# Performance work log

Measured on AMD Instinct MI355X. Metric: run time of the kernel, lower is better.

The kernel has to match this reference:

```python
import jax, jax.numpy as jnp
import numpy as np

IN_DIM = 256
OUT_DIM = 64   # per-head dim
NUM_HEADS = 8
B = 8
N = 1024


def setup_inputs() -> dict:
    key = jax.random.key(0)
    k_adj, k_h, kq, kk, kv, kbq, kbk, kbv = jax.random.split(key, 8)
    adj_matrix = jax.random.randint(k_adj, (N, N), 0, 2, dtype=jnp.int32)
    h = jax.random.normal(k_h, (B, N, IN_DIM), dtype=jnp.float32)
    s = 1.0 / np.sqrt(IN_DIM)
    Wq = jax.random.normal(kq, (IN_DIM, OUT_DIM * NUM_HEADS), dtype=jnp.float32) * s
    Wk = jax.random.normal(kk, (IN_DIM, OUT_DIM * NUM_HEADS), dtype=jnp.float32) * s
    Wv = jax.random.normal(kv, (IN_DIM, OUT_DIM * NUM_HEADS), dtype=jnp.float32) * s
    bq = jax.random.normal(kbq, (OUT_DIM * NUM_HEADS,), dtype=jnp.float32) * 0.01
    bk = jax.random.normal(kbk, (OUT_DIM * NUM_HEADS,), dtype=jnp.float32) * 0.01
    bv = jax.random.normal(kbv, (OUT_DIM * NUM_HEADS,), dtype=jnp.float32) * 0.01
    return {"adj_matrix": adj_matrix, "h": h, "Wq": Wq, "bq": bq,
            "Wk": Wk, "bk": bk, "Wv": Wv, "bv": bv}


def reference(adj_matrix, h, Wq, bq, Wk, bk, Wv, bv):
    B_, N_, _ = h.shape
    H, D = NUM_HEADS, OUT_DIM
    Qh = (h @ Wq + bq).reshape(B_, N_, H, D)
    Kh = (h @ Wk + bk).reshape(B_, N_, H, D)
    Vh = (h @ Wv + bv).reshape(B_, N_, H, D)
    scores = jnp.einsum('bnhd,bmhd->bhnm', Qh, Kh) / jnp.sqrt(jnp.float32(D))
    # adjacency mask broadcast over batch and heads (neigh_attention=True)
    scores = jnp.where(adj_matrix[None, None, :, :] == 0, -jnp.inf, scores)
    attn = jax.nn.softmax(scores, axis=-1)
    out = jnp.einsum('bhnm,bmhd->bnhd', attn, Vh)
    return out.reshape(B_, N_, H * D)
```

## Files before the change

### kernel.cpp

```cpp
#include <hip/hip_runtime.h>
#include <hip/hip_bf16.h>
#include <math.h>

#define IN_DIM 256
#define HD     512
#define NHEADS 8
#define DH     64
#define NSEQ   1024
#define BATCH  8

#define QSCALE 0.18033688011112042f

typedef unsigned short u16;
typedef unsigned int   u32;
typedef short bf16x8 __attribute__((ext_vector_type(8)));
typedef float f32x4  __attribute__((ext_vector_type(4)));
typedef float f32x16 __attribute__((ext_vector_type(16)));
typedef unsigned int u32x2 __attribute__((ext_vector_type(2)));

#if __has_builtin(__builtin_amdgcn_exp2f)
#define EXP2(x) __builtin_amdgcn_exp2f(x)
#else
#define EXP2(x) __expf(0.69314718056f * (x))
#endif

static __device__ __forceinline__ u16 f2bf(float x) {
    u32 u = __builtin_bit_cast(u32, x);
    u += 0x7FFFu + ((u >> 16) & 1u);
    return (u16)(u >> 16);
}
static __device__ __forceinline__ u32 pk(u16 a, u16 b) {
    return (u32)a | ((u32)b << 16);
}
static __device__ __forceinline__ u32 cvtpk(float a, float b) {
    __hip_bfloat162 t = __float22bfloat162_rn(make_float2(a, b));
    u32 r; __builtin_memcpy(&r, &t, 4);
    return r;
}
static __device__ __forceinline__ f32x16 maskinit(uint4 a, uint4 b) {
    f32x16 c;
    u32 ws[8] = {a.x, a.y, a.z, a.w, b.x, b.y, b.z, b.w};
#pragma unroll
    for (int i = 0; i < 8; ++i) {
        c[2 * i]     = __builtin_bit_cast(float, ws[i] << 16);
        c[2 * i + 1] = __builtin_bit_cast(float, ws[i] & 0xFFFF0000u);
    }
    return c;
}

static __device__ __forceinline__ void pswap(u32 &a, u32 &b) {
#if __has_builtin(__builtin_amdgcn_permlane32_swap)
    u32x2 r = __builtin_amdgcn_permlane32_swap(a, b, false, false);
    a = r.x; b = r.y;
#else
    const bool hi = (threadIdx.x & 32) != 0;
    u32 as = (u32)__shfl_xor((int)a, 32, 64);
    u32 bs = (u32)__shfl_xor((int)b, 32, 64);
    u32 na = hi ? bs : a;
    u32 nb = hi ? b  : as;
    a = na; b = nb;
#endif
}

#define MFMA32(a, b, c) __builtin_amdgcn_mfma_f32_32x32x16_bf16(a, b, c, 0, 0, 0)

#define GLOAD16(G, L)                                                          \
    __builtin_amdgcn_global_load_lds(                                          \
        (const __attribute__((address_space(1))) unsigned int*)(const void*)(G),\
        (__attribute__((address_space(3))) unsigned int*)(void*)(L), 16, 0, 0)

static __device__ __forceinline__ float sm_pack_half(const f32x16 st, bf16x8* pb) {
    float p[16];
#pragma unroll
    for (int r = 0; r < 16; ++r) p[r] = EXP2(st[r]);
    float t = (((p[0] + p[1]) + (p[2] + p[3])) + ((p[4] + p[5]) + (p[6] + p[7])))
            + (((p[8] + p[9]) + (p[10] + p[11])) + ((p[12] + p[13]) + (p[14] + p[15])));
    uint4 w0, w1;
    w0.x = cvtpk(p[0], p[1]);   w0.y = cvtpk(p[2], p[3]);
    w0.z = cvtpk(p[4], p[5]);   w0.w = cvtpk(p[6], p[7]);
    w1.x = cvtpk(p[8], p[9]);   w1.y = cvtpk(p[10], p[11]);
    w1.z = cvtpk(p[12], p[13]); w1.w = cvtpk(p[14], p[15]);
    pswap(w0.x, w1.x); pswap(w0.y, w1.y); pswap(w0.z, w1.z); pswap(w0.w, w1.w);
    pb[0] = __builtin_bit_cast(bf16x8, w0);
    pb[1] = __builtin_bit_cast(bf16x8, w1);
    return t;
}

__global__ __launch_bounds__(256)
void wtrans_kernel(const float* __restrict__ Wq, const float* __restrict__ Wk,
                   const float* __restrict__ Wv, u16* __restrict__ Wt)
{
    __shared__ float tile[64 * 65];
    const int bid = blockIdx.x, tid = threadIdx.x;
    const int k0 = (bid & 3) * 64, n0 = ((bid >> 2) & 7) * 64, wsel = bid >> 5;
    const float* W = (wsel == 0) ? Wq : (wsel == 1) ? Wk : Wv;
    u16* Out = Wt + (size_t)wsel * HD * IN_DIM;

    const int r = tid >> 2, c0 = (tid & 3) * 16;
#pragma unroll
    for (int j = 0; j < 16; j += 4) {
        float4 v = *(const float4*)(W + (size_t)(k0 + r) * HD + n0 + c0 + j);
        tile[r * 65 + c0 + j + 0] = v.x; tile[r * 65 + c0 + j + 1] = v.y;
        tile[r * 65 + c0 + j + 2] = v.z; tile[r * 65 + c0 + j + 3] = v.w;
    }
    __syncthreads();
    const int n = tid >> 2, ks = (tid & 3) * 16;
    u16 o[16];
#pragma unroll
    for (int j = 0; j < 16; ++j) o[j] = f2bf(tile[(ks + j) * 65 + n]);
    uint4 u0, u1;
    u0.x = pk(o[0], o[1]);   u0.y = pk(o[2], o[3]);
    u0.z = pk(o[4], o[5]);   u0.w = pk(o[6], o[7]);
    u1.x = pk(o[8], o[9]);   u1.y = pk(o[10], o[11]);
    u1.z = pk(o[12], o[13]); u1.w = pk(o[14], o[15]);
    u16* dst = Out + (size_t)(n0 + n) * IN_DIM + k0 + ks;
    *(uint4*)(dst) = u0;
    *(uint4*)(dst + 8) = u1;
}

__global__ __launch_bounds__(256, 4)
void gemm_mask_kernel(const float* __restrict__ h, const u16* __restrict__ Wt,
                      const int* __restrict__ adj,
                      const float* __restrict__ bq, const float* __restrict__ bk,
                      const float* __restrict__ bv,
                      u16* __restrict__ Qg, u16* __restrict__ Kg,
                      u16* __restrict__ Vtg, u16* __restrict__ Madd2)
{
    __shared__ u16 pool[64 * 64 + 3 * 64 * 64];
    const int tid = threadIdx.x;

    if (blockIdx.y >= 8) {
        int* tile = (int*)pool;
        const int abid = (blockIdx.y - 8) * 128 + blockIdx.x;
        const int tR = abid >> 4, tC = abid & 15;
        const int r = tid >> 2, cg = (tid & 3) * 16;
        const int* src = adj + (size_t)(tR * 64 + r) * NSEQ + tC * 64 + cg;
#pragma unroll
        for (int j = 0; j < 16; j += 4) {
            int4 a = *(const int4*)(src + j);
            tile[r * 65 + cg + j + 0] = a.x; tile[r * 65 + cg + j + 1] = a.y;
            tile[r * 65 + cg + j + 2] = a.z; tile[r * 65 + cg + j + 3] = a.w;
        }
        __syncthreads();
        const int q = tid >> 2, p0 = (tid & 3) * 16;
        u16 o[16];
#pragma unroll
        for (int j = 0; j < 16; ++j) {
            const int p = p0 + j;
            const int c = 32 * (p >> 5) + (p & 3) + 4 * ((p >> 4) & 1) + 8 * ((p >> 2) & 3);
            o[j] = (tile[q * 65 + c] == 0) ? (u16)0xFF7F : (u16)0;
        }
        uint4 u0, u1;
        u0.x = pk(o[0], o[1]);   u0.y = pk(o[2], o[3]);
        u0.z = pk(o[4], o[5]);   u0.w = pk(o[6], o[7]);
        u1.x = pk(o[8], o[9]);   u1.y = pk(o[10], o[11]);
        u1.z = pk(o[12], o[13]); u1.w = pk(o[14], o[15]);
        u16* dst = Madd2 + (size_t)(tR * 64 + q) * NSEQ + tC * 64 + p0;
        *(uint4*)(dst) = u0;
        *(uint4*)(dst + 8) = u1;
        return;
    }

    u16* As = pool;
    u16* Bs = pool + 64 * 64;

    const int m0 = blockIdx.x * 64;
    const int hh = blockIdx.y;
    const int n0 = hh * 64;

    const int w = tid >> 6, lane = tid & 63;
    const int l31 = lane & 31, half = lane >> 5;
    const int mh = w & 1, nh = w >> 1;
    const int s7 = l31 & 7;

    f32x16 acc[3] = {};

    const int arw = tid >> 2, acg = (tid & 3) * 2;
    const int brw = tid & 63, bgrp = tid >> 6;
    const float* srcA = h + (size_t)(m0 + arw) * IN_DIM;

    for (int kk = 0; kk < IN_DIM; kk += 64) {
        __syncthreads();
#pragma unroll
        for (int g = 0; g < 2; ++g) {
            const float* p = srcA + kk + (acg + g) * 8;
            float4 v0 = *(const float4*)(p);
            float4 v1 = *(const float4*)(p + 4);
            uint4 u;
            u.x = cvtpk(v0.x, v0.y); u.y = cvtpk(v0.z, v0.w);
            u.z = cvtpk(v1.x, v1.y); u.w = cvtpk(v1.z, v1.w);
            *(uint4*)&As[arw * 64 + (((acg + g) ^ (arw & 7)) * 8)] = u;
        }
#pragma unroll
        for (int i = 0; i < 6; ++i) {
            const int gc = bgrp * 6 + i;
            const int wh = gc >> 3, c8 = gc & 7;
            *(uint4*)&Bs[wh * 4096 + brw * 64 + ((c8 ^ (brw & 7)) * 8)] =
                *(const uint4*)(Wt + (size_t)wh * HD * IN_DIM +
                                (size_t)(n0 + brw) * IN_DIM + kk + c8 * 8);
        }
        __syncthreads();
        const int arow = (32 * mh + l31) * 64;
        const int brow = (32 * nh + l31) * 64;
#pragma unroll
        for (int s = 0; s < 4; ++s) {
            const int g = ((s * 2 + half) ^ s7) * 8;
            bf16x8 a = *(const bf16x8*)&As[arow + g];
#pragma unroll
            for (int wh = 0; wh < 3; ++wh) {
                bf16x8 b = *(const bf16x8*)&Bs[wh * 4096 + brow + g];
                acc[wh] = __builtin_amdgcn_mfma_f32_32x32x16_bf16(a, b, acc[wh], 0, 0, 0);
            }
        }
    }

    for (int which = 0; which < 2; ++which) {
        u16* T = pool;
        const float* bias = (which == 0) ? bq : bk;
        u16* Out = (which == 0) ? Qg : Kg;
        const float scale = (which == 0) ? QSCALE : 1.0f;
        const float bvv = bias[n0 + 32 * nh + l31];
        __syncthreads();
#pragma unroll
        for (int r = 0; r < 16; ++r) {
            const int row = 32 * mh + 4 * half + (r & 3) + 8 * (r >> 2);
            T[row * 72 + 32 * nh + l31] = f2bf((acc[which][r] + bvv) * scale);
        }
        __syncthreads();
        const int row = tid >> 2, qc = (tid & 3) * 16;
        u16* dst = Out + (size_t)(m0 + row) * HD + n0 + qc;
        const u16* srcT = &T[row * 72 + qc];
        *(uint4*)(dst)     = *(const uint4*)(srcT);
        *(uint4*)(dst + 8) = *(const uint4*)(srcT + 8);
    }

    {
        u16* T = pool;
        const int d = 32 * nh + l31;
        const float bvv = bv[n0 + d];
        __syncthreads();
#pragma unroll
        for (int g = 0; g < 4; ++g) {
            ushort4 o;
            o.x = f2bf(acc[2][4 * g + 0] + bvv);
            o.y = f2bf(acc[2][4 * g + 1] + bvv);
            o.z = f2bf(acc[2][4 * g + 2] + bvv);
            o.w = f2bf(acc[2][4 * g + 3] + bvv);
            *(ushort4*)&T[d * 72 + 32 * mh + 16 * half + 4 * g] = o;
        }
        __syncthreads();
        const int b = m0 >> 10, nloc = m0 & 1023;
        const int dd = tid >> 2, c = (tid & 3) * 16;
        u16* dst = Vtg + ((size_t)(b * NHEADS + hh) * DH + dd) * NSEQ + nloc + c;
        *(uint4*)(dst)     = *(uint4*)&T[dd * 72 + c];
        *(uint4*)(dst + 8) = *(uint4*)&T[dd * 72 + c + 8];
    }
}

__global__ __launch_bounds__(512, 4)
void attn_kernel(const u16* __restrict__ Madd2, const u16* __restrict__ Qg,
                 const u16* __restrict__ Kg, const u16* __restrict__ Vtg,
                 float* __restrict__ out)
{
    __shared__ __align__(16) u16 Ks[2][2][4096];
    __shared__ __align__(16) u16 Vs[2][2][4096];

    const int tid = threadIdx.x;
    const int w = tid >> 6, lane = tid & 63;
    const int team = w >> 2, j = w & 3;
    const int l31 = lane & 31, half = lane >> 5;
    const int bh = blockIdx.x, qt = blockIdx.y;
    const int b = bh >> 3;
    const int n0 = qt * 128;
    const size_t rowbase = (size_t)b * NSEQ;
    const int colbase = (bh & 7) * DH;
    const int q7 = l31 & 7;
    const int qA = j * 32 + l31;
    const int cbase = team * 8;

    const u16* qga = Qg + (rowbase + n0 + qA) * HD + colbase;
    bf16x8 qb[4];
#pragma unroll
    for (int s = 0; s < 4; ++s)
        qb[s] = *(const bf16x8*)(qga + s * 16 + half * 8);

    const int lrow = lane >> 3, lgran = (lane & 7) ^ lrow;
    const int br0 = j * 16, br1 = j * 16 + 8;
    const u16* kg0 = Kg + (rowbase + cbase * 64 + br0 + lrow) * HD + colbase + lgran * 8;
    const u16* kg1 = kg0 + (size_t)8 * HD;
    const u16* vg0 = Vtg + ((size_t)bh * DH + br0 + lrow) * NSEQ + cbase * 64 + lgran * 8;
    const u16* vg1 = vg0 + (size_t)8 * NSEQ;

#define STAGE(BUF, CH)                                                   \
    do {                                                                 \
        GLOAD16(kg0 + (size_t)(CH) * 64 * HD, &Ks[team][BUF][br0 * 64]); \
        GLOAD16(kg1 + (size_t)(CH) * 64 * HD, &Ks[team][BUF][br1 * 64]); \
        GLOAD16(vg0 + (CH) * 64,              &Vs[team][BUF][br0 * 64]); \
        GLOAD16(vg1 + (CH) * 64,              &Vs[team][BUF][br1 * 64]); \
    } while (0)

    const u16* mrow = Madd2 + (size_t)(n0 + qA) * NSEQ + cbase * 64 + half * 16;

    STAGE(0, 0);
    uint4 m0a = *(const uint4*)(mrow);
    uint4 m0b = *(const uint4*)(mrow + 8);
    uint4 m1a = *(const uint4*)(mrow + 32);
    uint4 m1b = *(const uint4*)(mrow + 40);
    __syncthreads();

    float l = 0.f;
    f32x16 O0 = {}, O1 = {};

    for (int ch = 0; ch < 8; ++ch) {
        const int cur = ch & 1;
        const u16* Kc = &Ks[team][cur][0];
        const u16* Vc = &Vs[team][cur][0];

        if (ch < 7) STAGE(1 - cur, ch + 1);

        f32x16 s0 = maskinit(m0a, m0b);
#pragma unroll
        for (int s = 0; s < 4; ++s) {
            const int g = ((s * 2 + half) ^ q7) * 8;
            bf16x8 ka = *(const bf16x8*)&Kc[l31 * 64 + g];
            s0 = MFMA32(ka, qb[s], s0);
        }
        bf16x8 pb[2];
        l += sm_pack_half(s0, pb);

#pragma unroll
        for (int s = 0; s < 2; ++s) {
            const int g = ((s * 2 + half) ^ q7) * 8;
            bf16x8 va0 = *(const bf16x8*)&Vc[l31 * 64 + g];
            bf16x8 va1 = *(const bf16x8*)&Vc[(32 + l31) * 64 + g];
            O0 = MFMA32(va0, pb[s], O0);
            O1 = MFMA32(va1, pb[s], O1);
        }

        f32x16 s1 = maskinit(m1a, m1b);
        if (ch < 7) {
            const u16* mn = mrow + (ch + 1) * 64;
            m0a = *(const uint4*)(mn);      m0b = *(const uint4*)(mn + 8);
            m1a = *(const uint4*)(mn + 32); m1b = *(const uint4*)(mn + 40);
        }
#pragma unroll
        for (int s = 0; s < 4; ++s) {
            const int g = ((s * 2 + half) ^ q7) * 8;
            bf16x8 ka = *(const bf16x8*)&Kc[(32 + l31) * 64 + g];
            s1 = MFMA32(ka, qb[s], s1);
        }
        l += sm_pack_half(s1, pb);

#pragma unroll
        for (int s = 2; s < 4; ++s) {
            const int g = ((s * 2 + half) ^ q7) * 8;
            bf16x8 va0 = *(const bf16x8*)&Vc[l31 * 64 + g];
            bf16x8 va1 = *(const bf16x8*)&Vc[(32 + l31) * 64 + g];
            O0 = MFMA32(va0, pb[s - 2], O0);
            O1 = MFMA32(va1, pb[s - 2], O1);
        }
        __syncthreads();
    }
#undef STAGE

    float4* Oex = (float4*)&Ks[0][0][0];
    float*  Lex = (float*)&Vs[0][0][0];

    if (team == 1) {
#pragma unroll
        for (int g = 0; g < 4; ++g) {
            float4 t;
            t.x = O0[4 * g + 0]; t.y = O0[4 * g + 1];
            t.z = O0[4 * g + 2]; t.w = O0[4 * g + 3];
            Oex[(j * 8 + g) * 64 + lane] = t;
            t.x = O1[4 * g + 0]; t.y = O1[4 * g + 1];
            t.z = O1[4 * g + 2]; t.w = O1[4 * g + 3];
            Oex[(j * 8 + 4 + g) * 64 + lane] = t;
        }
        Lex[j * 64 + lane] = l;
    }
    __syncthreads();
    if (team == 0) {
        l += Lex[j * 64 + lane];
#pragma unroll
        for (int g = 0; g < 4; ++g) {
            float4 t0 = Oex[(j * 8 + g) * 64 + lane];
            float4 t1 = Oex[(j * 8 + 4 + g) * 64 + lane];
            O0[4 * g + 0] += t0.x; O0[4 * g + 1] += t0.y;
            O0[4 * g + 2] += t0.z; O0[4 * g + 3] += t0.w;
            O1[4 * g + 0] += t1.x; O1[4 * g + 1] += t1.y;
            O1[4 * g + 2] += t1.z; O1[4 * g + 3] += t1.w;
        }

        l += __shfl_xor(l, 32, 64);
        const float inv = 1.0f / l;

        float* orow = out + (rowbase + n0 + qA) * HD + colbase;
#pragma unroll
        for (int g = 0; g < 4; ++g) {
            const int d0 = 4 * half + 8 * g;
            float4 a0, a1;
            a0.x = O0[4 * g + 0] * inv; a0.y = O0[4 * g + 1] * inv;
            a0.z = O0[4 * g + 2] * inv; a0.w = O0[4 * g + 3] * inv;
            a1.x = O1[4 * g + 0] * inv; a1.y = O1[4 * g + 1] * inv;
            a1.z = O1[4 * g + 2] * inv; a1.w = O1[4 * g + 3] * inv;
            *(float4*)(orow + d0)      = a0;
            *(float4*)(orow + 32 + d0) = a1;
        }
    }
}

extern "C" void kernel_launch(void* const* d_in, const int* in_sizes, int n_in,
                              void* d_out, int out_size, void* d_ws, size_t ws_size,
                              hipStream_t stream) {
    const int*   adj = (const int*)d_in[0];
    const float* h   = (const float*)d_in[1];
    const float* Wq  = (const float*)d_in[2];
    const float* bq  = (const float*)d_in[3];
    const float* Wk  = (const float*)d_in[4];
    const float* bk  = (const float*)d_in[5];
    const float* Wv  = (const float*)d_in[6];
    const float* bv  = (const float*)d_in[7];
    float* outp = (float*)d_out;

    u16* Wt    = (u16*)d_ws;
    u16* Qg    = Wt + (size_t)3 * HD * IN_DIM;
    u16* Kg    = Qg + (size_t)BATCH * NSEQ * HD;
    u16* Vtg   = Kg + (size_t)BATCH * NSEQ * HD;
    u16* Madd2 = Vtg + (size_t)BATCH * NSEQ * HD;
    (void)ws_size;

    wtrans_kernel<<<96, 256, 0, stream>>>(Wq, Wk, Wv, Wt);
    gemm_mask_kernel<<<dim3(BATCH * NSEQ / 64, 10), 256, 0, stream>>>(
        h, Wt, adj, bq, bk, bv, Qg, Kg, Vtg, Madd2);
    attn_kernel<<<dim3(BATCH * NHEADS, NSEQ / 128), 512, 0, stream>>>(
        Madd2, Qg, Kg, Vtg, outp);
}
```

Before: 132.1 us.

## Pre-convert h to bf16 and double-buffer QKV GEMM with direct global-to-LDS loads

The h-to-bf16 conversion moves into the weight-transpose kernel, which gains 128 extra blocks that write a bf16 copy of h to workspace. The QKV projection GEMM then stages A and B tiles with GLOAD16 (presumably global-to-LDS direct loads) into a double-buffered LDS layout, prefetching the next K slice while MFMAs run on the current one. This is meant to hide global load latency and remove per-iteration register staging and conversion. In exchange, LDS per block grows to 64KB, occupancy drops (launch bounds 4 to 2), and there is an extra pass over h through workspace.

```diff
diff --git a/kernel.cpp b/kernel.cpp
--- a/kernel.cpp
+++ b/kernel.cpp
@@ -88,10 +88,28 @@
 
 __global__ __launch_bounds__(256)
 void wtrans_kernel(const float* __restrict__ Wq, const float* __restrict__ Wk,
-                   const float* __restrict__ Wv, u16* __restrict__ Wt)
+                   const float* __restrict__ Wv, const float* __restrict__ h,
+                   u16* __restrict__ Wt, u16* __restrict__ hb)
 {
     __shared__ float tile[64 * 65];
     const int bid = blockIdx.x, tid = threadIdx.x;
+
+    if (bid >= 96) {
+        const int ab = bid - 96;
+        const float4* hs = (const float4*)h;
+        uint2* hd = (uint2*)hb;
+        const int base = ab * 4096 + tid;
+#pragma unroll
+        for (int j = 0; j < 16; ++j) {
+            float4 v = hs[base + j * 256];
+            uint2 o;
+            o.x = cvtpk(v.x, v.y);
+            o.y = cvtpk(v.z, v.w);
+            hd[base + j * 256] = o;
+        }
+        return;
+    }
+
     const int k0 = (bid & 3) * 64, n0 = ((bid >> 2) & 7) * 64, wsel = bid >> 5;
     const float* W = (wsel == 0) ? Wq : (wsel == 1) ? Wk : Wv;
     u16* Out = Wt + (size_t)wsel * HD * IN_DIM;
@@ -118,19 +136,19 @@
     *(uint4*)(dst + 8) = u1;
 }
 
-__global__ __launch_bounds__(256, 4)
-void gemm_mask_kernel(const float* __restrict__ h, const u16* __restrict__ Wt,
+__global__ __launch_bounds__(256, 2)
+void gemm_mask_kernel(const u16* __restrict__ hb, const u16* __restrict__ Wt,
                       const int* __restrict__ adj,
                       const float* __restrict__ bq, const float* __restrict__ bk,
                       const float* __restrict__ bv,
                       u16* __restrict__ Qg, u16* __restrict__ Kg,
                       u16* __restrict__ Vtg, u16* __restrict__ Madd2)
 {
-    __shared__ u16 pool[64 * 64 + 3 * 64 * 64];
+    __shared__ __align__(16) u16 lds[32768];
     const int tid = threadIdx.x;
 
     if (blockIdx.y >= 8) {
-        int* tile = (int*)pool;
+        int* tile = (int*)lds;
         const int abid = (blockIdx.y - 8) * 128 + blockIdx.x;
         const int tR = abid >> 4, tC = abid & 15;
         const int r = tid >> 2, cg = (tid & 3) * 16;
@@ -161,9 +179,6 @@
         return;
     }
 
-    u16* As = pool;
-    u16* Bs = pool + 64 * 64;
-
     const int m0 = blockIdx.x * 64;
     const int hh = blockIdx.y;
     const int n0 = hh * 64;
@@ -173,49 +188,52 @@
     const int mh = w & 1, nh = w >> 1;
     const int s7 = l31 & 7;
 
+    const int lrow = lane >> 3, lgran = (lane & 7) ^ lrow;
+    const int r0 = w * 16;
+    const u16* ag = hb + (size_t)(m0 + r0 + lrow) * IN_DIM + lgran * 8;
+    const u16* bg = Wt + (size_t)(n0 + r0 + lrow) * IN_DIM + lgran * 8;
+
+#define STAGE_G(BUF, KK)                                                        \
+    do {                                                                        \
+        u16* a0 = lds + (BUF) * 4096 + r0 * 64;                                 \
+        u16* b0 = lds + 8192 + (BUF) * 12288 + r0 * 64;                         \
+        GLOAD16(ag + (KK) * 64,                                    a0);         \
+        GLOAD16(ag + (KK) * 64 + 8 * IN_DIM,                       a0 + 512);   \
+        GLOAD16(bg + (KK) * 64,                                    b0);         \
+        GLOAD16(bg + (KK) * 64 + 8 * IN_DIM,                       b0 + 512);   \
+        GLOAD16(bg + (KK) * 64 + (size_t)HD * IN_DIM,              b0 + 4096);  \
+        GLOAD16(bg + (KK) * 64 + (size_t)HD * IN_DIM + 8 * IN_DIM, b0 + 4608);  \
+        GLOAD16(bg + (KK) * 64 + (size_t)2 * HD * IN_DIM,          b0 + 8192);  \
+        GLOAD16(bg + (KK) * 64 + (size_t)2 * HD * IN_DIM + 8 * IN_DIM, b0 + 8704); \
+    } while (0)
+
     f32x16 acc[3] = {};
-
-    const int arw = tid >> 2, acg = (tid & 3) * 2;
-    const int brw = tid & 63, bgrp = tid >> 6;
-    const float* srcA = h + (size_t)(m0 + arw) * IN_DIM;
-
-    for (int kk = 0; kk < IN_DIM; kk += 64) {
-        __syncthreads();
-#pragma unroll
-        for (int g = 0; g < 2; ++g) {
-            const float* p = srcA + kk + (acg + g) * 8;
-            float4 v0 = *(const float4*)(p);
-            float4 v1 = *(const float4*)(p + 4);
-            uint4 u;
-            u.x = cvtpk(v0.x, v0.y); u.y = cvtpk(v0.z, v0.w);
-            u.z = cvtpk(v1.x, v1.y); u.w = cvtpk(v1.z, v1.w);
-            *(uint4*)&As[arw * 64 + (((acg + g) ^ (arw & 7)) * 8)] = u;
-        }
-#pragma unroll
-        for (int i = 0; i < 6; ++i) {
-            const int gc = bgrp * 6 + i;
-            const int wh = gc >> 3, c8 = gc & 7;
-            *(uint4*)&Bs[wh * 4096 + brw * 64 + ((c8 ^ (brw & 7)) * 8)] =
-                *(const uint4*)(Wt + (size_t)wh * HD * IN_DIM +
-                                (size_t)(n0 + brw) * IN_DIM + kk + c8 * 8);
-        }
-        __syncthreads();
-        const int arow = (32 * mh + l31) * 64;
-        const int brow = (32 * nh + l31) * 64;
+    const int arow = (32 * mh + l31) * 64;
+    const int brow = (32 * nh + l31) * 64;
+
+    STAGE_G(0, 0);
+#pragma unroll
+    for (int kk = 0; kk < 4; ++kk) {
+        const int cur = kk & 1;
+        __syncthreads();
+        if (kk < 3) STAGE_G(1 - cur, kk + 1);
+        const u16* Ac = lds + cur * 4096;
+        const u16* Bc = lds + 8192 + cur * 12288;
 #pragma unroll
         for (int s = 0; s < 4; ++s) {
             const int g = ((s * 2 + half) ^ s7) * 8;
-            bf16x8 a = *(const bf16x8*)&As[arow + g];
+            bf16x8 a = *(const bf16x8*)&Ac[arow + g];
 #pragma unroll
             for (int wh = 0; wh < 3; ++wh) {
-                bf16x8 b = *(const bf16x8*)&Bs[wh * 4096 + brow + g];
+                bf16x8 b = *(const bf16x8*)&Bc[wh * 4096 + brow + g];
                 acc[wh] = __builtin_amdgcn_mfma_f32_32x32x16_bf16(a, b, acc[wh], 0, 0, 0);
             }
         }
     }
+#undef STAGE_G
 
     for (int which = 0; which < 2; ++which) {
-        u16* T = pool;
+        u16* T = lds;
         const float* bias = (which == 0) ? bq : bk;
         u16* Out = (which == 0) ? Qg : Kg;
         const float scale = (which == 0) ? QSCALE : 1.0f;
@@ -235,7 +253,7 @@
     }
 
     {
-        u16* T = pool;
+        u16* T = lds;
         const int d = 32 * nh + l31;
         const float bvv = bv[n0 + d];
         __syncthreads();
@@ -428,11 +446,12 @@
     u16* Kg    = Qg + (size_t)BATCH * NSEQ * HD;
     u16* Vtg   = Kg + (size_t)BATCH * NSEQ * HD;
     u16* Madd2 = Vtg + (size_t)BATCH * NSEQ * HD;
+    u16* hb    = Madd2 + (size_t)NSEQ * NSEQ;
     (void)ws_size;
 
-    wtrans_kernel<<<96, 256, 0, stream>>>(Wq, Wk, Wv, Wt);
+    wtrans_kernel<<<224, 256, 0, stream>>>(Wq, Wk, Wv, h, Wt, hb);
     gemm_mask_kernel<<<dim3(BATCH * NSEQ / 64, 10), 256, 0, stream>>>(
-        h, Wt, adj, bq, bk, bv, Qg, Kg, Vtg, Madd2);
+        hb, Wt, adj, bq, bk, bv, Qg, Kg, Vtg, Madd2);
     attn_kernel<<<dim3(BATCH * NHEADS, NSEQ / 128), 512, 0, stream>>>(
         Madd2, Qg, Kg, Vtg, outp);
 }
```

New measurement: 124.5 us. 1.06x faster.
